# Kernel tuning notes

Measured on AMD Instinct MI355X. Metric: run time of the kernel, lower is better.

The kernel has to match this reference:

```python
import jax, jax.numpy as jnp
import numpy as np

N, CIN, T, V, P, K, NCLS = 8, 3, 300, 25, 3, 9, 60
EPS = 1e-5


def setup_inputs() -> dict:
    key = jax.random.key(0)
    ks = jax.random.split(key, 10)
    rn = lambda k, s: jax.random.normal(k, s, jnp.float32) * 0.05
    return {
        "x": jax.random.normal(ks[0], (N, CIN, T, V), jnp.float32),
        "A": jax.random.uniform(ks[1], (P, V, V), jnp.float32),
        "bn_in_g": jnp.ones((V * CIN,), jnp.float32),
        "bn_in_b": jnp.zeros((V * CIN,), jnp.float32),
        "fin_W": rn(ks[2], (64, CIN)), "fin_b": jnp.zeros((64,), jnp.float32),
        "imp0": jnp.ones((V, V), jnp.float32), "imp1": jnp.ones((V, V), jnp.float32),
        "imp2": jnp.ones((V, V), jnp.float32), "imp3": jnp.ones((V, V), jnp.float32),
        "W0": rn(ks[3], (64 * P, 64)), "g0": jnp.ones((64,), jnp.float32), "b0": jnp.zeros((64,), jnp.float32),
        "W1": rn(ks[4], (128 * P, 64)), "g1": jnp.ones((128,), jnp.float32), "b1": jnp.zeros((128,), jnp.float32),
        "Wr1": rn(ks[5], (128, 64)), "gr1": jnp.ones((128,), jnp.float32), "br1": jnp.zeros((128,), jnp.float32),
        "W2": rn(ks[6], (256 * P, 128)), "g2": jnp.ones((256,), jnp.float32), "b2": jnp.zeros((256,), jnp.float32),
        "Wr2": rn(ks[7], (256, 128)), "gr2": jnp.ones((256,), jnp.float32), "br2": jnp.zeros((256,), jnp.float32),
        "W3": rn(ks[8], (256 * P, 256)), "g3": jnp.ones((256,), jnp.float32), "b3": jnp.zeros((256,), jnp.float32),
        "fout_W": rn(ks[9], (NCLS, 256)), "fout_b": jnp.zeros((NCLS,), jnp.float32),
    }


def _bn(x, g, b, axes):
    # training-mode batchnorm (batch statistics), matching nn.BatchNorm in train()
    m = jnp.mean(x, axes, keepdims=True)
    v = jnp.var(x, axes, keepdims=True)
    return (x - m) * jax.lax.rsqrt(v + EPS) * g + b


def _lt_matrix(t):
    # lower-triangular-style shift matrix: lt[r, c] = 1 iff 0 <= c - r < K (stride 1)
    d = jnp.arange(t)[None, :] - jnp.arange(t)[:, None]
    return ((d >= 0) & (d < K)).astype(jnp.float32)


def _layer(x, A, W, g, b, lt, res, final_relu):
    # x: (N, Cin, T, V); W: (P*Cout, Cin); A: (P, V, V); lt: (T, T)
    n, _, t, v = x.shape
    cout = W.shape[0] // P
    y = jnp.einsum('nctv,kc->nktv', x, W).reshape(n, P, cout, t, v)   # 1x1 conv + split/stack
    z = jnp.einsum('npctv,pvw->npctw', y, A)                          # spatial graph matmul
    u = jnp.einsum('npctv,ts->npcsv', z, lt)                          # dense LxL temporal matmul
    h = u.sum(1)                                                      # sum over partitions -> (N, Cout, T, V)
    h = jax.nn.relu(_bn(h, g[None, :, None, None], b[None, :, None, None], (0, 2, 3)))
    out = h + res
    return jax.nn.relu(out) if final_relu else out


def reference(x, A, bn_in_g, bn_in_b, fin_W, fin_b, imp0, imp1, imp2, imp3,
              W0, g0, b0, W1, g1, b1, Wr1, gr1, br1,
              W2, g2, b2, Wr2, gr2, br2, W3, g3, b3, fout_W, fout_b):
    n, c, t, v = x.shape
    # input BatchNorm1d over (V*C) channels
    xp = x.transpose(0, 3, 1, 2).reshape(n, v * c, t)
    xp = _bn(xp, bn_in_g[None, :, None], bn_in_b[None, :, None], (0, 2))
    h = xp.reshape(n, v, c, t).transpose(0, 2, 3, 1)                  # (N, C, T, V)
    h = jnp.einsum('nctv,oc->notv', h, fin_W) + fin_b[None, :, None, None]
    lt = _lt_matrix(t)
    # layer 0: no residual, no final relu (Dropout only, p=0 -> identity)
    h = _layer(h, A * imp0, W0, g0, b0, lt, 0.0, False)
    # layer 1: 64 -> 128, conv+BN residual
    r1 = _bn(jnp.einsum('nctv,oc->notv', h, Wr1), gr1[None, :, None, None], br1[None, :, None, None], (0, 2, 3))
    h = _layer(h, A * imp1, W1, g1, b1, lt, r1, True)
    # layer 2: 128 -> 256, conv+BN residual
    r2 = _bn(jnp.einsum('nctv,oc->notv', h, Wr2), gr2[None, :, None, None], br2[None, :, None, None], (0, 2, 3))
    h = _layer(h, A * imp2, W2, g2, b2, lt, r2, True)
    # layer 3: 256 -> 256, identity residual
    h = _layer(h, A * imp3, W3, g3, b3, lt, h, True)
    # average pool over joints, 1x1 classification conv
    h = h.mean(-1, keepdims=True)                                     # (N, 256, T, 1)
    out = jnp.einsum('nctv,oc->notv', h, fout_W) + fout_b[None, :, None, None]
    return out[..., 0]                                                # (N, num_classes, T)
```

## Files before the change

kernel.cpp:

```cpp
#include <hip/hip_runtime.h>

#define EPS 1e-5f
typedef unsigned short u16;
typedef __attribute__((ext_vector_type(8))) short short8;
typedef __attribute__((ext_vector_type(4))) float f32x4;

__device__ __forceinline__ float bf2f(u16 u) {
  union { unsigned int i; float f; } c; c.i = ((unsigned int)u) << 16; return c.f;
}
__device__ __forceinline__ u16 f2bf(float f) {
  union { float f; unsigned int i; } c; c.f = f;
  unsigned int u = c.i;
  u += 0x7fffu + ((u >> 16) & 1u);
  return (u16)(u >> 16);
}
__device__ __forceinline__ unsigned int cvt_pk_bf16(float lo, float hi) {
  unsigned int r;
  asm("v_cvt_pk_bf16_f32 %0, %1, %2" : "=v"(r) : "v"(lo), "v"(hi));
  return r;
}
__device__ __forceinline__ short8 load8u(const u16* p) {
  short8 v; __builtin_memcpy(&v, p, 16); return v;
}
__device__ __forceinline__ void gload16(const u16* g, u16* l) {
  __builtin_amdgcn_global_load_lds(
      (__attribute__((address_space(1))) void*)(void*)g,
      (__attribute__((address_space(3))) void*)l, 16, 0, 0);
}

__device__ __forceinline__ void prep_w_elem(const float* W, u16* Wt,
    int cin, int cout, int P, int idx) {
  const int K = P*cin;
  const int co = idx / K, k = idx % K;
  const int p = k / cin, ci = k % cin;
  Wt[idx] = f2bf(W[((size_t)(p*cout + co))*cin + ci]);
}

__global__ __launch_bounds__(256) void k_prep_all(
    const float* __restrict__ A,
    const float* __restrict__ i0, const float* __restrict__ i1,
    const float* __restrict__ i2, const float* __restrict__ i3,
    const float* __restrict__ W0, const float* __restrict__ W1,
    const float* __restrict__ Wr1, const float* __restrict__ W2,
    const float* __restrict__ Wr2, const float* __restrict__ W3,
    u16* W0t, u16* W1t, u16* Wr1t, u16* W2t,
    u16* Wr2t, u16* W3t, u16* ATb, u16* hpad) {
  int idx = blockIdx.x*256 + threadIdx.x;
  if (idx < 12288) { prep_w_elem(W0,  W0t,  64,  64,  3, idx); return; }
  idx -= 12288;
  if (idx < 24576) { prep_w_elem(W1,  W1t,  64,  128, 3, idx); return; }
  idx -= 24576;
  if (idx < 8192)  { prep_w_elem(Wr1, Wr1t, 64,  128, 1, idx); return; }
  idx -= 8192;
  if (idx < 98304) { prep_w_elem(W2,  W2t,  128, 256, 3, idx); return; }
  idx -= 98304;
  if (idx < 32768) { prep_w_elem(Wr2, Wr2t, 128, 256, 1, idx); return; }
  idx -= 32768;
  if (idx < 196608){ prep_w_elem(W3,  W3t,  256, 256, 3, idx); return; }
  idx -= 196608;
  if (idx < 12288) {
    const int l = idx / 3072, r = idx % 3072;
    const int p = r / 1024, wv = r % 1024;
    const int w = wv >> 5, v = wv & 31;
    float val = 0.f;
    if (w < 25 && v < 25) {
      const float* imp = (l==0)?i0:(l==1)?i1:(l==2)?i2:i3;
      val = A[(p*25 + v)*25 + w] * imp[v*25 + w];
    }
    ATb[idx] = f2bf(val);
    return;
  }
  idx -= 12288;
  if (idx < 32) hpad[idx] = 0;
}

__global__ __launch_bounds__(256) void k_bn_in_stats(const float* __restrict__ x,
    const float* __restrict__ g, const float* __restrict__ b,
    float* __restrict__ iscale, float* __restrict__ ishift) {
  const int j = blockIdx.x;
  const int c = j % 3, v = j / 3;
  const int tid = threadIdx.x;
  float s = 0.f, q = 0.f;
  for (int i = tid; i < 2400; i += 256) {
    const int n = i / 300, t = i % 300;
    const float val = x[(((size_t)n*3 + c)*300 + t)*25 + v];
    s += val; q += val*val;
  }
  __shared__ float rs[256], rq[256];
  rs[tid] = s; rq[tid] = q;
  __syncthreads();
  for (int off = 128; off > 0; off >>= 1) {
    if (tid < off) { rs[tid] += rs[tid+off]; rq[tid] += rq[tid+off]; }
    __syncthreads();
  }
  if (tid == 0) {
    const float mean = rs[0] / 2400.f;
    const float var  = rq[0] / 2400.f - mean*mean;
    const float sc = g[j] * rsqrtf(var + EPS);
    iscale[j] = sc;
    ishift[j] = b[j] - mean*sc;
  }
}

__global__ __launch_bounds__(256) void k_fin(const float* __restrict__ x,
    const float* __restrict__ iscale, const float* __restrict__ ishift,
    const float* __restrict__ fW, const float* __restrict__ fb,
    u16* __restrict__ H) {
  const int n = blockIdx.y;
  const int t0 = blockIdx.x * 10;
  const int tid = threadIdx.x;
  __shared__ float xn[3][250];
  __shared__ float wsh[64][3];
  __shared__ float bsh[64];
  if (tid < 192) wsh[tid/3][tid%3] = fW[tid];
  if (tid < 64)  bsh[tid] = fb[tid];
  for (int i = tid; i < 750; i += 256) {
    const int c = i / 250, pos = i % 250;
    const int t = t0 + pos/25, v = pos%25;
    const int j = v*3 + c;
    xn[c][pos] = x[(((size_t)n*3 + c)*300 + t)*25 + v] * iscale[j] + ishift[j];
  }
  __syncthreads();
  for (int e = tid; e < 64*250; e += 256) {
    const int o = e / 250, pos = e % 250;
    float acc = bsh[o]
              + xn[0][pos]*wsh[o][0] + xn[1][pos]*wsh[o][1] + xn[2][pos]*wsh[o][2];
    const int t = t0 + pos/25, v = pos%25;
    H[(((size_t)n*64 + o)*300 + t)*25 + v] = f2bf(acc);
  }
}

__global__ __launch_bounds__(256) void k_hmk(const u16* __restrict__ H,
    u16* __restrict__ Hmk, int cin) {
  const int m0  = blockIdx.x * 64;
  const int ci0 = blockIdx.y * 32;
  const int n   = blockIdx.z;
  __shared__ u16 tile[32][72];
  const int tid = threadIdx.x;
  {
    const int ci = tid >> 3, chunk = tid & 7;
    const int m = m0 + chunk * 8;
    const u16* src = &H[(size_t)(n*cin + ci0 + ci)*7500];
    short8 v;
    if (m + 7 < 7500) {
      v = load8u(&src[m]);
    } else {
      #pragma unroll
      for (int j = 0; j < 8; ++j)
        ((u16*)&v)[j] = (m + j < 7500) ? src[m + j] : (u16)0;
    }
    *(short8*)&tile[ci][chunk*8] = v;
  }
  __syncthreads();
  const int mr = tid >> 2, cq = (tid & 3) * 8;
  const int m = m0 + mr;
  if (m < 7500) {
    short8 v;
    #pragma unroll
    for (int j = 0; j < 8; ++j) ((u16*)&v)[j] = tile[cq + j][mr];
    *(short8*)&Hmk[((size_t)n*7500 + m)*cin + ci0 + cq] = v;
  }
}

__global__ __launch_bounds__(256) void k_xa_mfma(const u16* __restrict__ H,
    const u16* __restrict__ ATl, u16* __restrict__ XA, int cin, int K) {
  const int lane = threadIdx.x & 63, wid = threadIdx.x >> 6;
  const int t = blockIdx.x * 4 + wid;
  const int n = blockIdx.y;
  const int lrow = lane & 15, lchunk = lane >> 4;
  short8 bf[3][2];
  #pragma unroll
  for (int p = 0; p < 3; ++p)
    #pragma unroll
    for (int wt = 0; wt < 2; ++wt)
      bf[p][wt] = *(const short8*)&ATl[(p*32 + wt*16 + lrow)*32 + lchunk*8];
  const int ntile = cin >> 4;
  const size_t mrow0 = ((size_t)n*300 + t)*25;
  const int ciq = lchunk*4;
  for (int citile = 0; citile < ntile; ++citile) {
    const int ci = citile*16 + lrow;
    const short8 af = load8u(&H[((size_t)(n*cin + ci)*300 + t)*25 + lchunk*8]);
    #pragma unroll
    for (int p = 0; p < 3; ++p) {
      #pragma unroll
      for (int wt = 0; wt < 2; ++wt) {
        f32x4 acc = (f32x4){0.f, 0.f, 0.f, 0.f};
        acc = __builtin_amdgcn_mfma_f32_16x16x32_bf16(af, bf[p][wt], acc, 0, 0, 0);
        const int w = wt*16 + lrow;
        if (w < 25) {
          uint2 pk;
          pk.x = cvt_pk_bf16(acc[0], acc[1]);
          pk.y = cvt_pk_bf16(acc[2], acc[3]);
          *(uint2*)&XA[(mrow0 + w)*K + p*cin + citile*16 + ciq] = pk;
        }
      }
    }
  }
}

__global__ __launch_bounds__(256) void k_gemm(const u16* __restrict__ Asrc,
    const u16* __restrict__ Bsrc, u16* __restrict__ Cb, int K) {
  const int n0b = blockIdx.x * 64;
  const int m0  = blockIdx.y * 128;
  const int tid = threadIdx.x;
  const int lane = tid & 63, wid = tid >> 6;
  const int wm = (wid & 1) * 64, wn = (wid >> 1) * 32;

  __shared__ u16 As[128*64];
  __shared__ u16 Bs[64*64];

  f32x4 acc[4][2];
  #pragma unroll
  for (int mi = 0; mi < 4; ++mi)
    #pragma unroll
    for (int ni = 0; ni < 2; ++ni) acc[mi][ni] = (f32x4){0.f,0.f,0.f,0.f};

  const int rA = tid >> 3, cA = tid & 7;

  const int nkt = K >> 6;
  for (int kt = 0; kt < nkt; ++kt) {
    const int kbase = kt * 64;
    __syncthreads();
    #pragma unroll
    for (int i = 0; i < 4; ++i) {
      const int idx = tid + i*256;
      const int r = rA + i*32;
      int m = m0 + r; if (m > 59999) m = 59999;
      gload16(Asrc + (size_t)m*K + kbase + ((cA ^ (r & 7)) * 8), &As[idx*8]);
    }
    #pragma unroll
    for (int i = 0; i < 2; ++i) {
      const int idx = tid + i*256;
      const int r = rA + i*32;
      gload16(Bsrc + (size_t)(n0b + r)*K + kbase + ((cA ^ (r & 7)) * 8), &Bs[idx*8]);
    }
    __syncthreads();
    #pragma unroll
    for (int kc = 0; kc < 2; ++kc) {
      const int kchunk = kc*4 + (lane >> 4);
      short8 a[4], b[2];
      #pragma unroll
      for (int mi = 0; mi < 4; ++mi) {
        const int m = wm + mi*16 + (lane & 15);
        a[mi] = *(const short8*)&As[m*64 + ((kchunk ^ (m & 7)) * 8)];
      }
      #pragma unroll
      for (int ni = 0; ni < 2; ++ni) {
        const int r = wn + ni*16 + (lane & 15);
        b[ni] = *(const short8*)&Bs[r*64 + ((kchunk ^ (r & 7)) * 8)];
      }
      #pragma unroll
      for (int mi = 0; mi < 4; ++mi)
        #pragma unroll
        for (int ni = 0; ni < 2; ++ni)
          acc[mi][ni] = __builtin_amdgcn_mfma_f32_16x16x32_bf16(a[mi], b[ni], acc[mi][ni], 0, 0, 0);
    }
  }

  const int mrow = (lane >> 4) * 4;
  #pragma unroll
  for (int mi = 0; mi < 4; ++mi) {
    const int mb = m0 + wm + mi*16 + mrow;
    if (mb >= 60000) continue;
    #pragma unroll
    for (int ni = 0; ni < 2; ++ni) {
      const int co = n0b + wn + ni*16 + (lane & 15);
      uint2 pk;
      pk.x = cvt_pk_bf16(acc[mi][ni][0], acc[mi][ni][1]);
      pk.y = cvt_pk_bf16(acc[mi][ni][2], acc[mi][ni][3]);
      *(uint2*)&Cb[(size_t)co*60000 + mb] = pk;
    }
  }
}

__global__ __launch_bounds__(512) void k_gemm2(const u16* __restrict__ Asrc,
    const u16* __restrict__ Bsrc, u16* __restrict__ Cb, int K) {
  const int m0 = blockIdx.x * 128;
  const int tid = threadIdx.x;
  const int lane = tid & 63, wid = tid >> 6;
  const int wm = (wid >> 2) * 64, wn = (wid & 3) * 64;

  __shared__ u16 As[128*64];
  __shared__ u16 Bs[256*64];

  f32x4 acc[4][4];
  #pragma unroll
  for (int mi = 0; mi < 4; ++mi)
    #pragma unroll
    for (int ni = 0; ni < 4; ++ni) acc[mi][ni] = (f32x4){0.f,0.f,0.f,0.f};

  const int rA = tid >> 3, cA = tid & 7;

  const int nkt = K >> 6;
  for (int kt = 0; kt < nkt; ++kt) {
    const int kbase = kt * 64;
    __syncthreads();
    #pragma unroll
    for (int i = 0; i < 2; ++i) {
      const int idx = tid + i*512;
      const int r = rA + i*64;
      int m = m0 + r; if (m > 59999) m = 59999;
      gload16(Asrc + (size_t)m*K + kbase + ((cA ^ (r & 7)) * 8), &As[idx*8]);
    }
    #pragma unroll
    for (int i = 0; i < 4; ++i) {
      const int idx = tid + i*512;
      const int r = rA + i*64;
      gload16(Bsrc + (size_t)r*K + kbase + ((cA ^ (r & 7)) * 8), &Bs[idx*8]);
    }
    __syncthreads();
    #pragma unroll
    for (int kc = 0; kc < 2; ++kc) {
      const int kchunk = kc*4 + (lane >> 4);
      short8 a[4], b[4];
      #pragma unroll
      for (int mi = 0; mi < 4; ++mi) {
        const int m = wm + mi*16 + (lane & 15);
        a[mi] = *(const short8*)&As[m*64 + ((kchunk ^ (m & 7)) * 8)];
      }
      #pragma unroll
      for (int ni = 0; ni < 4; ++ni) {
        const int r = wn + ni*16 + (lane & 15);
        b[ni] = *(const short8*)&Bs[r*64 + ((kchunk ^ (r & 7)) * 8)];
      }
      #pragma unroll
      for (int mi = 0; mi < 4; ++mi)
        #pragma unroll
        for (int ni = 0; ni < 4; ++ni)
          acc[mi][ni] = __builtin_amdgcn_mfma_f32_16x16x32_bf16(a[mi], b[ni], acc[mi][ni], 0, 0, 0);
    }
  }

  const int mrow = (lane >> 4) * 4;
  #pragma unroll
  for (int mi = 0; mi < 4; ++mi) {
    const int mb = m0 + wm + mi*16 + mrow;
    if (mb >= 60000) continue;
    #pragma unroll
    for (int ni = 0; ni < 4; ++ni) {
      const int co = wn + ni*16 + (lane & 15);
      uint2 pk;
      pk.x = cvt_pk_bf16(acc[mi][ni][0], acc[mi][ni][1]);
      pk.y = cvt_pk_bf16(acc[mi][ni][2], acc[mi][ni][3]);
      *(uint2*)&Cb[(size_t)co*60000 + mb] = pk;
    }
  }
}

__global__ __launch_bounds__(256) void k_bn_part_win(const u16* __restrict__ G,
    float* __restrict__ part, int cout) {
  const int c = blockIdx.x, n = blockIdx.y;
  const int tid = threadIdx.x;
  const u16* gb = G + (size_t)c*60000 + (size_t)n*7500;
  float s = 0.f, q = 0.f;
  for (int i = tid; i < 7500; i += 256) {
    const int ss = i / 25, w = i % 25;
    float S = 0.f;
    if (ss >= 8) {
      #pragma unroll
      for (int d = 0; d < 9; ++d) S += bf2f(gb[i - d*25]);
    } else {
      for (int tt = 0; tt <= ss; ++tt) S += bf2f(gb[tt*25 + w]);
    }
    s += S; q += S*S;
  }
  __shared__ float rs[256], rq[256];
  rs[tid] = s; rq[tid] = q;
  __syncthreads();
  for (int off = 128; off > 0; off >>= 1) {
    if (tid < off) { rs[tid] += rs[tid+off]; rq[tid] += rq[tid+off]; }
    __syncthreads();
  }
  if (tid == 0) {
    part[((size_t)c*8 + n)*2]     = rs[0];
    part[((size_t)c*8 + n)*2 + 1] = rq[0];
  }
}

__global__ __launch_bounds__(256) void k_bn_part_plain(const u16* __restrict__ R,
    float* __restrict__ part, int cout) {
  const int c = blockIdx.x, n = blockIdx.y;
  const int tid = threadIdx.x;
  const u16* rb = R + (size_t)c*60000 + (size_t)n*7500;
  float s = 0.f, q = 0.f;
  for (int i = tid; i < 7500; i += 256) {
    const float val = bf2f(rb[i]);
    s += val; q += val*val;
  }
  __shared__ float rs[256], rq[256];
  rs[tid] = s; rq[tid] = q;
  __syncthreads();
  for (int off = 128; off > 0; off >>= 1) {
    if (tid < off) { rs[tid] += rs[tid+off]; rq[tid] += rq[tid+off]; }
    __syncthreads();
  }
  if (tid == 0) {
    part[((size_t)c*8 + n)*2]     = rs[0];
    part[((size_t)c*8 + n)*2 + 1] = rq[0];
  }
}

__global__ __launch_bounds__(256) void k_apply2(const u16* __restrict__ G,
    const u16* __restrict__ Rb, const u16* Hres,
    const float* __restrict__ part, const float* __restrict__ g, const float* __restrict__ b,
    const float* __restrict__ rpart, const float* __restrict__ rg, const float* __restrict__ rbb,
    u16* Out, int cout, int mode) {
  const int bc = blockIdx.x;
  const int c = bc % cout, n = bc / cout;
  float s = 0.f, q = 0.f;
  #pragma unroll
  for (int i = 0; i < 8; ++i) {
    s += part[((size_t)c*8 + i)*2];
    q += part[((size_t)c*8 + i)*2 + 1];
  }
  const float mean = s / 60000.f;
  const float var  = q / 60000.f - mean*mean;
  const float sc = g[c] * rsqrtf(var + EPS);
  const float sh = b[c] - mean*sc;
  float rsc = 0.f, rsh = 0.f;
  if (mode == 1) {
    float s2 = 0.f, q2 = 0.f;
    #pragma unroll
    for (int i = 0; i < 8; ++i) {
      s2 += rpart[((size_t)c*8 + i)*2];
      q2 += rpart[((size_t)c*8 + i)*2 + 1];
    }
    const float m2 = s2 / 60000.f;
    const float v2 = q2 / 60000.f - m2*m2;
    rsc = rg[c] * rsqrtf(v2 + EPS);
    rsh = rbb[c] - m2*rsc;
  }
  const u16* gb = G + (size_t)c*60000 + (size_t)n*7500;
  const size_t rbase = (size_t)c*60000 + (size_t)n*7500;
  for (int i = threadIdx.x; i < 7500; i += 256) {
    const int ss = i / 25, w = i % 25;
    float S = 0.f;
    if (ss >= 8) {
      #pragma unroll
      for (int d = 0; d < 9; ++d) S += bf2f(gb[i - d*25]);
    } else {
      for (int tt = 0; tt <= ss; ++tt) S += bf2f(gb[tt*25 + w]);
    }
    const float h = fmaxf(S*sc + sh, 0.f);
    float o;
    if (mode == 0)      o = h;
    else if (mode == 1) o = fmaxf(h + (bf2f(Rb[rbase + i])*rsc + rsh), 0.f);
    else                o = fmaxf(h + bf2f(Hres[(size_t)bc*7500 + i]), 0.f);
    Out[(size_t)bc*7500 + i] = f2bf(o);
  }
}

__global__ void k_pool(const u16* __restrict__ H, float* __restrict__ HP) {
  const int idx = blockIdx.x*256 + threadIdx.x;
  if (idx >= 8*256*300) return;
  const u16* base = H + (size_t)idx * 25;
  float s = 0.f;
  #pragma unroll
  for (int v = 0; v < 25; ++v) s += bf2f(base[v]);
  HP[idx] = s * (1.f/25.f);
}

__global__ __launch_bounds__(256) void k_fout(const float* __restrict__ HP,
    const float* __restrict__ fW, const float* __restrict__ fb,
    float* __restrict__ out) {
  const int n = blockIdx.y;
  const int t0 = blockIdx.x * 32;
  const int tid = threadIdx.x;
  __shared__ float hp[256][32];
  for (int i = tid; i < 256*32; i += 256) {
    const int c = i / 32, tt = i % 32;
    const int t = t0 + tt;
    hp[c][tt] = (t < 300) ? HP[((size_t)n*256 + c)*300 + t] : 0.f;
  }
  __syncthreads();
  for (int e = tid; e < 60*32; e += 256) {
    const int o = e / 32, tt = e % 32;
    const int t = t0 + tt;
    if (t >= 300) continue;
    float acc = fb[o];
    for (int c = 0; c < 256; ++c) acc += hp[c][tt] * fW[o*256 + c];
    out[((size_t)n*60 + o)*300 + t] = acc;
  }
}

extern "C" void kernel_launch(void* const* d_in, const int* in_sizes, int n_in,
                              void* d_out, int out_size, void* d_ws, size_t ws_size,
                              hipStream_t stream) {
  (void)in_sizes; (void)n_in; (void)out_size; (void)ws_size;
  const float* x     = (const float*)d_in[0];
  const float* A     = (const float*)d_in[1];
  const float* bng   = (const float*)d_in[2];
  const float* bnb   = (const float*)d_in[3];
  const float* finW  = (const float*)d_in[4];
  const float* finb  = (const float*)d_in[5];
  const float* imp0  = (const float*)d_in[6];
  const float* imp1  = (const float*)d_in[7];
  const float* imp2  = (const float*)d_in[8];
  const float* imp3  = (const float*)d_in[9];
  const float* W0    = (const float*)d_in[10];
  const float* g0    = (const float*)d_in[11];
  const float* b0    = (const float*)d_in[12];
  const float* W1    = (const float*)d_in[13];
  const float* g1    = (const float*)d_in[14];
  const float* b1    = (const float*)d_in[15];
  const float* Wr1   = (const float*)d_in[16];
  const float* gr1   = (const float*)d_in[17];
  const float* br1   = (const float*)d_in[18];
  const float* W2    = (const float*)d_in[19];
  const float* g2    = (const float*)d_in[20];
  const float* b2    = (const float*)d_in[21];
  const float* Wr2   = (const float*)d_in[22];
  const float* gr2   = (const float*)d_in[23];
  const float* br2   = (const float*)d_in[24];
  const float* W3    = (const float*)d_in[25];
  const float* g3    = (const float*)d_in[26];
  const float* b3    = (const float*)d_in[27];
  const float* foutW = (const float*)d_in[28];
  const float* foutb = (const float*)d_in[29];
  float* out = (float*)d_out;

  char* base = (char*)d_ws;
  u16*   Z    = (u16*)base;
  u16*   Hmk  = (u16*)base;
  float* HP   = (float*)(base + 40000000);
  float* PART = (float*)(base + 45000000);
  float* RPART= (float*)(base + 45100000);
  u16*   XA   = (u16*)(base + 61440000);
  u16*   Rb   = (u16*)(base + 107520000);
  u16*   Hct  = (u16*)(base + 153600000);
  u16*   HPAD = (u16*)(base + 184320000);
  u16*   ATb  = (u16*)(base + 185000000);
  u16*   WT   = (u16*)(base + 186777600);
  float* ST   = (float*)(base + 188000000);
  float* ISC = ST, *ISH = ST + 80;

  u16* W0t  = WT;
  u16* W1t  = WT + 12288;
  u16* Wr1t = WT + 36864;
  u16* W2t  = WT + 45056;
  u16* Wr2t = WT + 143360;
  u16* W3t  = WT + 176128;

  k_prep_all<<<1505, 256, 0, stream>>>(A, imp0, imp1, imp2, imp3,
      W0, W1, Wr1, W2, Wr2, W3, W0t, W1t, Wr1t, W2t, Wr2t, W3t, ATb, HPAD);

  k_bn_in_stats<<<75, 256, 0, stream>>>(x, bng, bnb, ISC, ISH);
  k_fin<<<dim3(30, 8), 256, 0, stream>>>(x, ISC, ISH, finW, finb, Hct);

  const int MT = 469;

  k_xa_mfma<<<dim3(75, 8), 256, 0, stream>>>(Hct, ATb, XA, 64, 192);
  k_gemm<<<dim3(1, MT), 256, 0, stream>>>(XA, W0t, Z, 192);
  k_bn_part_win<<<dim3(64, 8), 256, 0, stream>>>(Z, PART, 64);
  k_apply2<<<8*64, 256, 0, stream>>>(Z, nullptr, nullptr, PART, g0, b0,
      nullptr, nullptr, nullptr, Hct, 64, 0);

  k_hmk<<<dim3(118, 2, 8), 256, 0, stream>>>(Hct, Hmk, 64);
  k_xa_mfma<<<dim3(75, 8), 256, 0, stream>>>(Hct, ATb + 1*3072, XA, 64, 192);
  k_gemm<<<dim3(2, MT), 256, 0, stream>>>(Hmk, Wr1t, Rb, 64);
  k_bn_part_plain<<<dim3(128, 8), 256, 0, stream>>>(Rb, RPART, 128);
  k_gemm<<<dim3(2, MT), 256, 0, stream>>>(XA, W1t, Z, 192);
  k_bn_part_win<<<dim3(128, 8), 256, 0, stream>>>(Z, PART, 128);
  k_apply2<<<8*128, 256, 0, stream>>>(Z, Rb, nullptr, PART, g1, b1,
      RPART, gr1, br1, Hct, 128, 1);

  k_hmk<<<dim3(118, 4, 8), 256, 0, stream>>>(Hct, Hmk, 128);
  k_xa_mfma<<<dim3(75, 8), 256, 0, stream>>>(Hct, ATb + 2*3072, XA, 128, 384);
  k_gemm2<<<MT, 512, 0, stream>>>(Hmk, Wr2t, Rb, 128);
  k_bn_part_plain<<<dim3(256, 8), 256, 0, stream>>>(Rb, RPART, 256);
  k_gemm2<<<MT, 512, 0, stream>>>(XA, W2t, Z, 384);
  k_bn_part_win<<<dim3(256, 8), 256, 0, stream>>>(Z, PART, 256);
  k_apply2<<<8*256, 256, 0, stream>>>(Z, Rb, nullptr, PART, g2, b2,
      RPART, gr2, br2, Hct, 256, 1);

  k_xa_mfma<<<dim3(75, 8), 256, 0, stream>>>(Hct, ATb + 3*3072, XA, 256, 768);
  k_gemm2<<<MT, 512, 0, stream>>>(XA, W3t, Z, 768);
  k_bn_part_win<<<dim3(256, 8), 256, 0, stream>>>(Z, PART, 256);
  k_apply2<<<8*256, 256, 0, stream>>>(Z, nullptr, Hct, PART, g3, b3,
      nullptr, nullptr, nullptr, Hct, 256, 2);

  k_pool<<<2400, 256, 0, stream>>>(Hct, HP);
  k_fout<<<dim3(10, 8), 256, 0, stream>>>(HP, foutW, foutb, out);
}
```

Before: 473.7 us.

## Stage graph-mixing output in shared memory for coalesced row writes

Rewrites the A-mixing MFMA kernel so each block handles a single (n, t) slice, spreads the (partition, channel-tile) chunks across its four waves, and stages the results in LDS. Whole 25-row output rows of XA are then written back with contiguous 16-byte stores, replacing scattered 8-byte writes. This trades an LDS round trip, a barrier, scalar 2-byte LDS stores and reloading the A fragments per chunk for better global write coalescing and more blocks.

```diff
diff --git a/kernel.cpp b/kernel.cpp
--- a/kernel.cpp
+++ b/kernel.cpp
@@ -162,39 +162,38 @@
   }
 }
 
-__global__ __launch_bounds__(256) void k_xa_mfma(const u16* __restrict__ H,
+__global__ __launch_bounds__(256) void k_xa_mfma2(const u16* __restrict__ H,
     const u16* __restrict__ ATl, u16* __restrict__ XA, int cin, int K) {
-  const int lane = threadIdx.x & 63, wid = threadIdx.x >> 6;
-  const int t = blockIdx.x * 4 + wid;
-  const int n = blockIdx.y;
+  const int t = blockIdx.x, n = blockIdx.y;
+  const int tid = threadIdx.x, lane = tid & 63, wid = tid >> 6;
   const int lrow = lane & 15, lchunk = lane >> 4;
-  short8 bf[3][2];
-  #pragma unroll
-  for (int p = 0; p < 3; ++p)
-    #pragma unroll
-    for (int wt = 0; wt < 2; ++wt)
-      bf[p][wt] = *(const short8*)&ATl[(p*32 + wt*16 + lrow)*32 + lchunk*8];
-  const int ntile = cin >> 4;
-  const size_t mrow0 = ((size_t)n*300 + t)*25;
-  const int ciq = lchunk*4;
-  for (int citile = 0; citile < ntile; ++citile) {
+  extern __shared__ u16 zt[];
+  const int ldz = K + 8;
+  const int ncit = cin >> 4;
+  const int nchunks = 3 * ncit;
+  for (int ch = wid; ch < nchunks; ch += 4) {
+    const int p = ch / ncit, citile = ch % ncit;
     const int ci = citile*16 + lrow;
     const short8 af = load8u(&H[((size_t)(n*cin + ci)*300 + t)*25 + lchunk*8]);
-    #pragma unroll
-    for (int p = 0; p < 3; ++p) {
-      #pragma unroll
-      for (int wt = 0; wt < 2; ++wt) {
-        f32x4 acc = (f32x4){0.f, 0.f, 0.f, 0.f};
-        acc = __builtin_amdgcn_mfma_f32_16x16x32_bf16(af, bf[p][wt], acc, 0, 0, 0);
-        const int w = wt*16 + lrow;
-        if (w < 25) {
-          uint2 pk;
-          pk.x = cvt_pk_bf16(acc[0], acc[1]);
-          pk.y = cvt_pk_bf16(acc[2], acc[3]);
-          *(uint2*)&XA[(mrow0 + w)*K + p*cin + citile*16 + ciq] = pk;
-        }
+    const int col = p*cin + citile*16 + lrow;
+    #pragma unroll
+    for (int wt = 0; wt < 2; ++wt) {
+      const short8 bf = *(const short8*)&ATl[(p*32 + wt*16 + lrow)*32 + lchunk*8];
+      f32x4 acc = (f32x4){0.f, 0.f, 0.f, 0.f};
+      acc = __builtin_amdgcn_mfma_f32_16x16x32_bf16(bf, af, acc, 0, 0, 0);
+      #pragma unroll
+      for (int r = 0; r < 4; ++r) {
+        const int w = wt*16 + lchunk*4 + r;
+        if (w < 25) zt[w*ldz + col] = f2bf(acc[r]);
       }
     }
+  }
+  __syncthreads();
+  const int rowchunks = K >> 3;
+  const size_t mbase = ((size_t)n*300 + t)*25;
+  for (int i = tid; i < 25*rowchunks; i += 256) {
+    const int row = i / rowchunks, c = i % rowchunks;
+    *(short8*)&XA[(mbase + row)*K + c*8] = *(const short8*)&zt[row*ldz + c*8];
   }
 }
 
@@ -548,15 +547,18 @@
   k_fin<<<dim3(30, 8), 256, 0, stream>>>(x, ISC, ISH, finW, finb, Hct);
 
   const int MT = 469;
-
-  k_xa_mfma<<<dim3(75, 8), 256, 0, stream>>>(Hct, ATb, XA, 64, 192);
+  const int ldsK192 = (192 + 8) * 25 * 2;
+  const int ldsK384 = (384 + 8) * 25 * 2;
+  const int ldsK768 = (768 + 8) * 25 * 2;
+
+  k_xa_mfma2<<<dim3(300, 8), 256, ldsK192, stream>>>(Hct, ATb, XA, 64, 192);
   k_gemm<<<dim3(1, MT), 256, 0, stream>>>(XA, W0t, Z, 192);
   k_bn_part_win<<<dim3(64, 8), 256, 0, stream>>>(Z, PART, 64);
   k_apply2<<<8*64, 256, 0, stream>>>(Z, nullptr, nullptr, PART, g0, b0,
       nullptr, nullptr, nullptr, Hct, 64, 0);
 
   k_hmk<<<dim3(118, 2, 8), 256, 0, stream>>>(Hct, Hmk, 64);
-  k_xa_mfma<<<dim3(75, 8), 256, 0, stream>>>(Hct, ATb + 1*3072, XA, 64, 192);
+  k_xa_mfma2<<<dim3(300, 8), 256, ldsK192, stream>>>(Hct, ATb + 1*3072, XA, 64, 192);
   k_gemm<<<dim3(2, MT), 256, 0, stream>>>(Hmk, Wr1t, Rb, 64);
   k_bn_part_plain<<<dim3(128, 8), 256, 0, stream>>>(Rb, RPART, 128);
   k_gemm<<<dim3(2, MT), 256, 0, stream>>>(XA, W1t, Z, 192);
@@ -565,7 +567,7 @@
       RPART, gr1, br1, Hct, 128, 1);
 
   k_hmk<<<dim3(118, 4, 8), 256, 0, stream>>>(Hct, Hmk, 128);
-  k_xa_mfma<<<dim3(75, 8), 256, 0, stream>>>(Hct, ATb + 2*3072, XA, 128, 384);
+  k_xa_mfma2<<<dim3(300, 8), 256, ldsK384, stream>>>(Hct, ATb + 2*3072, XA, 128, 384);
   k_gemm2<<<MT, 512, 0, stream>>>(Hmk, Wr2t, Rb, 128);
   k_bn_part_plain<<<dim3(256, 8), 256, 0, stream>>>(Rb, RPART, 256);
   k_gemm2<<<MT, 512, 0, stream>>>(XA, W2t, Z, 384);
@@ -573,7 +575,7 @@
   k_apply2<<<8*256, 256, 0, stream>>>(Z, Rb, nullptr, PART, g2, b2,
       RPART, gr2, br2, Hct, 256, 1);
 
-  k_xa_mfma<<<dim3(75, 8), 256, 0, stream>>>(Hct, ATb + 3*3072, XA, 256, 768);
+  k_xa_mfma2<<<dim3(300, 8), 256, ldsK768, stream>>>(Hct, ATb + 3*3072, XA, 256, 768);
   k_gemm2<<<MT, 512, 0, stream>>>(XA, W3t, Z, 768);
   k_bn_part_win<<<dim3(256, 8), 256, 0, stream>>>(Z, PART, 256);
   k_apply2<<<8*256, 256, 0, stream>>>(Z, nullptr, Hct, PART, g3, b3,
```

Measured after the change: 501.6 us. 5.9% more time.
